# Kernel optimization log

Hardware: AMD Instinct MI355X
Metric: run time of the kernel (lower is better)

## Reference

```python
import jax, jax.numpy as jnp
import numpy as np

EPS = 1e-5
NUM_GROUPS = 32


def setup_inputs() -> dict:
    key = jax.random.key(0)
    ks = jax.random.split(key, 8)
    B, C, H, W = 4, 256, 64, 64
    cond_dim = 512
    s = 0.02
    return {
        "x": jax.random.normal(ks[0], (B, C, H, W), jnp.float32),
        "cond": jax.random.normal(ks[1], (B, cond_dim), jnp.float32),
        "lin_w": jax.random.normal(ks[2], (cond_dim, 2 * C), jnp.float32) * s,
        "lin_b": jnp.zeros((2 * C,), jnp.float32),
        "qkv_w": jax.random.normal(ks[3], (C, 3 * C), jnp.float32) * s,
        "qkv_b": jnp.zeros((3 * C,), jnp.float32),
        "proj_w": jax.random.normal(ks[4], (C, C), jnp.float32) * s,
        "proj_b": jnp.zeros((C,), jnp.float32),
    }


def _group_norm(x):
    # x: [B, C, H, W]; normalize per (batch, group) over (C/G, H, W)
    B, C, H, W = x.shape
    xg = x.reshape(B, NUM_GROUPS, C // NUM_GROUPS, H, W)
    mean = jnp.mean(xg, axis=(2, 3, 4), keepdims=True)
    var = jnp.var(xg, axis=(2, 3, 4), keepdims=True)
    xg = (xg - mean) * jax.lax.rsqrt(var + EPS)
    return xg.reshape(B, C, H, W)


def reference(x, cond, lin_w, lin_b, qkv_w, qkv_b, proj_w, proj_b):
    B, C, H, W = x.shape
    # AdaGroupNorm
    h = _group_norm(x)
    sb = cond @ lin_w + lin_b                       # [B, 2C]
    scale, bias = jnp.split(sb, 2, axis=-1)
    h = h * (1.0 + scale)[:, :, None, None] + bias[:, :, None, None]
    # tokens: [B, HW, C]
    t = h.reshape(B, C, H * W).transpose(0, 2, 1)
    qkv = t @ qkv_w + qkv_b                          # [B, HW, 3C]
    q, k, v = jnp.split(qkv, 3, axis=-1)
    attn = jnp.einsum("bnc,bmc->bnm", q, k) / jnp.sqrt(jnp.float32(C))
    attn = jax.nn.softmax(attn, axis=-1)
    o = jnp.einsum("bnm,bmc->bnc", attn, v)          # [B, HW, C]
    o = o @ proj_w + proj_b
    o = o.transpose(0, 2, 1).reshape(B, C, H, W)
    return x + o
```

## Files before the change

kernel.cpp:

```cpp
#include <hip/hip_runtime.h>
#include <stdint.h>


#define AS1 __attribute__((address_space(1)))
#define AS3 __attribute__((address_space(3)))

typedef __attribute__((ext_vector_type(8))) short bf16x8;
typedef __attribute__((ext_vector_type(16))) float f32x16;

static __device__ __forceinline__ unsigned short bf16r(float x) {
  union { float f; unsigned u; } v; v.f = x;
  return (unsigned short)((v.u + 0x7fffu + ((v.u >> 16) & 1u)) >> 16);
}
static __device__ __forceinline__ float bf2f(short x) {
  union { unsigned u; float f; } v;
  v.u = ((unsigned)(unsigned short)x) << 16;
  return v.f;
}
static __device__ __forceinline__ unsigned bf16pack(float lo, float hi) {
  union { float f; unsigned u; } a, b; a.f = lo; b.f = hi;
  unsigned ua = a.u + 0x7fffu + ((a.u >> 16) & 1u);
  unsigned ub = b.u + 0x7fffu + ((b.u >> 16) & 1u);
  return (ua >> 16) | (ub & 0xffff0000u);
}
static __device__ __forceinline__ void gload16(const void* g, void* lds_uniform) {
  __builtin_amdgcn_global_load_lds((const AS1 unsigned*)g, (AS3 unsigned*)lds_uniform,
                                   16, 0, 0);
}
static __device__ __forceinline__ f32x16 mfma_bf16(bf16x8 a, bf16x8 b, f32x16 c) {
  return __builtin_amdgcn_mfma_f32_32x32x16_bf16(a, b, c, 0, 0, 0);
}

__global__ __launch_bounds__(256) void prep_kernel(
    const float* __restrict__ qkv_w, const float* __restrict__ proj_w,
    const float* __restrict__ cond, const float* __restrict__ lin_w,
    const float* __restrict__ lin_b,
    unsigned short* __restrict__ qkvwT, unsigned short* __restrict__ projwT,
    float* __restrict__ sb) {
  int bid = blockIdx.x, t = threadIdx.x;
  if (bid < 64) {
    __shared__ float tile[64][68];
    const float* src;
    unsigned short* dst;
    int srcCols, j0, c0;
    if (bid < 48) {
      src = qkv_w; dst = qkvwT; srcCols = 768;
      j0 = (bid >> 2) * 64; c0 = (bid & 3) * 64;
    } else {
      int b2 = bid - 48;
      src = proj_w; dst = projwT; srcCols = 256;
      j0 = (b2 >> 2) * 64; c0 = (b2 & 3) * 64;
    }
    int r = t >> 4, col4 = (t & 15) * 4;
#pragma unroll
    for (int q = 0; q < 4; ++q) {
      float4 v = *(const float4*)(src + (size_t)(c0 + r + q * 16) * srcCols + j0 + col4);
      *(float4*)&tile[r + q * 16][col4] = v;
    }
    __syncthreads();
    int jj = t >> 2, cc = (t & 3) * 16;
    union { unsigned short us[16]; bf16x8 v[2]; } o;
#pragma unroll
    for (int i = 0; i < 16; ++i) o.us[i] = bf16r(tile[cc + i][jj]);
    unsigned short* dp = dst + (size_t)(j0 + jj) * 256 + c0 + cc;
    *(bf16x8*)dp = o.v[0];
    *(bf16x8*)(dp + 8) = o.v[1];
  } else {
    int s = bid - 64;
    int b = s >> 1, j = (s & 1) * 256 + t;
    float acc = lin_b[j];
    const float* cp = cond + b * 512;
    const float* wp = lin_w + j;
#pragma unroll 8
    for (int kk = 0; kk < 512; ++kk) acc += cp[kk] * wp[(size_t)kk * 512];
    sb[b * 512 + j] = acc;
  }
}

__global__ __launch_bounds__(256) void gn_stats_kernel(
    const float* __restrict__ x, float* __restrict__ stats) {
  int bg = blockIdx.x;
  const float* p = x + (size_t)bg * 32768;
  float s = 0.f, ss = 0.f;
  for (int k = 0; k < 32; ++k) {
    int i = threadIdx.x * 4 + k * 1024;
    float4 v = *(const float4*)(p + i);
    s += v.x + v.y + v.z + v.w;
    ss += v.x * v.x + v.y * v.y + v.z * v.z + v.w * v.w;
  }
#pragma unroll
  for (int off = 1; off < 64; off <<= 1) {
    s += __shfl_xor(s, off, 64);
    ss += __shfl_xor(ss, off, 64);
  }
  __shared__ float red[8];
  if ((threadIdx.x & 63) == 0) {
    red[(threadIdx.x >> 6) * 2] = s;
    red[(threadIdx.x >> 6) * 2 + 1] = ss;
  }
  __syncthreads();
  if (threadIdx.x == 0) {
    float S = 0.f, SS = 0.f;
#pragma unroll
    for (int i = 0; i < 4; ++i) { S += red[i * 2]; SS += red[i * 2 + 1]; }
    float mean = S * (1.f / 32768.f);
    float var = SS * (1.f / 32768.f) - mean * mean;
    stats[bg * 2] = mean;
    stats[bg * 2 + 1] = rsqrtf(var + 1e-5f);
  }
}

__global__ __launch_bounds__(256) void gn_apply_kernel(
    const float* __restrict__ x, const float* __restrict__ stats,
    const float* __restrict__ sb, unsigned short* __restrict__ ht) {
  __shared__ __align__(16) unsigned short tile[64][72];
  int b = blockIdx.x >> 8, cb = (blockIdx.x >> 6) & 3, nb = blockIdx.x & 63;
  int t = threadIdx.x;
  int c0 = cb * 64, n0 = nb * 64;
#pragma unroll
  for (int q = 0; q < 4; ++q) {
    int r = q * 16 + (t >> 4);
    int nn = (t & 15) * 4;
    int c = c0 + r;
    float mean = stats[(b * 32 + (c >> 3)) * 2];
    float rstd = stats[(b * 32 + (c >> 3)) * 2 + 1];
    float scl = sb[b * 512 + c], bia = sb[b * 512 + 256 + c];
    float A = rstd * (1.f + scl);
    float Bp = bia - mean * A;
    float4 v = *(const float4*)(x + ((size_t)(b * 256 + c)) * 4096 + n0 + nn);
    ushort4 pk;
    pk.x = bf16r(v.x * A + Bp);
    pk.y = bf16r(v.y * A + Bp);
    pk.z = bf16r(v.z * A + Bp);
    pk.w = bf16r(v.w * A + Bp);
    *(ushort4*)&tile[r][nn] = pk;
  }
  __syncthreads();
#pragma unroll
  for (int q = 0; q < 2; ++q) {
    int n = t & 63, cbase = (t >> 6) * 8 + q * 32;
    bf16x8 outv;
#pragma unroll
    for (int j = 0; j < 8; ++j) outv[j] = (short)tile[cbase + j][n];
    *(bf16x8*)(ht + ((size_t)(b * 4096 + n0 + n)) * 256 + c0 + cbase) = outv;
  }
}

__global__ __launch_bounds__(256, 2) void qkv_gemm_kernel(
    const unsigned short* __restrict__ ht, const unsigned short* __restrict__ wT,
    const float* __restrict__ qkv_b, unsigned short* __restrict__ q_buf,
    unsigned short* __restrict__ k_buf, unsigned short* __restrict__ vt_buf) {
  __shared__ __align__(16) unsigned short lA[8192];
  __shared__ __align__(16) unsigned short lB[8192];
  int bid = blockIdx.x;
  int b = bid / 192, rem = bid % 192;
  int m0 = (rem / 6) * 128, j0 = (rem % 6) * 128;
  int tid = threadIdx.x, lane = tid & 63, w = tid >> 6;
  int wm = w >> 1, wn = w & 1, l31 = lane & 31, lh = lane >> 5;

  f32x16 acc[2][2];
#pragma unroll
  for (int i = 0; i < 2; ++i)
#pragma unroll
    for (int jj = 0; jj < 2; ++jj) acc[i][jj] = (f32x16)0.f;

  const char* htg = (const char*)ht;
  const char* wtg = (const char*)wT;

  for (int ks = 0; ks < 4; ++ks) {
    int k0 = ks * 64;
    if (ks) __syncthreads();
#pragma unroll
    for (int i = 0; i < 4; ++i) {
      int obase = (w * 4 + i) * 1024;
      int o = obase + lane * 16;
      int row = o >> 7, colb = o & 127;
      int sw = (row & 7) << 4;
      gload16(htg + (((size_t)(b * 4096 + m0 + row)) * 256 + k0) * 2 + (colb ^ sw),
              (char*)lA + obase);
      gload16(wtg + (((size_t)(j0 + row)) * 256 + k0) * 2 + (colb ^ sw),
              (char*)lB + obase);
    }
    __syncthreads();
#pragma unroll
    for (int ks16 = 0; ks16 < 4; ++ks16) {
      int colb = ks16 * 32 + lh * 16;
      bf16x8 af[2], bf[2];
#pragma unroll
      for (int ms = 0; ms < 2; ++ms) {
        int row = wm * 64 + ms * 32 + l31;
        af[ms] = *(const bf16x8*)((const char*)lA + row * 128 + (colb ^ ((row & 7) << 4)));
      }
#pragma unroll
      for (int ns = 0; ns < 2; ++ns) {
        int row = wn * 64 + ns * 32 + l31;
        bf[ns] = *(const bf16x8*)((const char*)lB + row * 128 + (colb ^ ((row & 7) << 4)));
      }
#pragma unroll
      for (int ms = 0; ms < 2; ++ms)
#pragma unroll
        for (int ns = 0; ns < 2; ++ns) acc[ms][ns] = mfma_bf16(af[ms], bf[ns], acc[ms][ns]);
    }
  }

#pragma unroll
  for (int ms = 0; ms < 2; ++ms)
#pragma unroll
    for (int ns = 0; ns < 2; ++ns) {
      int j = j0 + wn * 64 + ns * 32 + l31;
      float bias = qkv_b[j];
      if (j < 512) {
        unsigned short* dst = (j < 256) ? q_buf : k_buf;
        int jj = j & 255;
#pragma unroll
        for (int r = 0; r < 16; ++r) {
          int mrow = m0 + wm * 64 + ms * 32 + (r & 3) + 8 * (r >> 2) + 4 * lh;
          dst[((size_t)(b * 4096) + mrow) * 256 + jj] = bf16r(acc[ms][ns][r] + bias);
        }
      } else {
        int d = j - 512;
#pragma unroll
        for (int qd = 0; qd < 4; ++qd) {
          int nbase = m0 + wm * 64 + ms * 32 + 8 * qd + 4 * lh;
          ushort4 pk;
          pk.x = bf16r(acc[ms][ns][qd * 4 + 0] + bias);
          pk.y = bf16r(acc[ms][ns][qd * 4 + 1] + bias);
          pk.z = bf16r(acc[ms][ns][qd * 4 + 2] + bias);
          pk.w = bf16r(acc[ms][ns][qd * 4 + 3] + bias);
          *(ushort4*)(vt_buf + ((size_t)(b * 256) + d) * 4096 + nbase) = pk;
        }
      }
    }
}

__global__ __launch_bounds__(512, 2) void flash_kernel(
    const unsigned short* __restrict__ qb, const unsigned short* __restrict__ kb,
    const unsigned short* __restrict__ vtb, unsigned short* __restrict__ op0,
    unsigned short* __restrict__ op1, float* __restrict__ lbuf) {
  __shared__ __align__(16) char lds[131072];
  int bid = blockIdx.x;
  int b = (bid & 7) >> 1;
  int kvh = bid & 1;
  int qt = bid >> 3;
  int tid = threadIdx.x, lane = tid & 63, w = tid >> 6;
  int wq = w & 3, wk = w >> 2;
  int l31 = lane & 31, lh = lane >> 5;
  const size_t bq = (size_t)b * 4096;
  const int qrow = qt * 128 + wq * 32 + l31;

  bf16x8 qf[16];
  const unsigned short* qp = qb + (bq + qrow) * 256;
#pragma unroll
  for (int f = 0; f < 16; ++f) qf[f] = *(const bf16x8*)(qp + f * 16 + lh * 8);

  f32x16 oacc[8];
#pragma unroll
  for (int dt = 0; dt < 8; ++dt) oacc[dt] = (f32x16)0.f;
  float l = 0.f;

  const char* kg = (const char*)(kb + (bq + (size_t)kvh * 2048) * 256);
  const char* vg = (const char*)(vtb + (size_t)b * 1048576 + (size_t)kvh * 2048);
  const float sc = 0.09016844f;

  auto STAGE = [&](int bufsel, int it2) {
    char* base = lds + bufsel * 65536;
    int key0 = it2 * 64;
#pragma unroll
    for (int i = 0; i < 8; ++i) {
      int obase = w * 8192 + i * 1024;
      int o = obase + lane * 16;
      if (w < 4) {
        int row = o >> 9, colb = o & 511;
        gload16(kg + (size_t)(key0 + row) * 512 + (colb ^ ((row & 7) << 4)),
                base + obase);
      } else {
        int vo = o - 32768;
        int rd = vo >> 7, cb2 = vo & 127;
        gload16(vg + (size_t)rd * 8192 + key0 * 2 + (cb2 ^ ((rd & 7) << 4)),
                base + obase);
      }
    }
  };

  STAGE(0, 0);
  __syncthreads();

  for (int it = 0; it < 32; ++it) {
    int cur = it & 1;
    if (it < 31) STAGE(cur ^ 1, it + 1);
    char* kbase = lds + cur * 65536;
    char* vbase = kbase + 32768;

    f32x16 sa = (f32x16)0.f;
#pragma unroll
    for (int cc = 0; cc < 16; ++cc) {
      int row = wk * 32 + l31;
      int colb = cc * 32 + lh * 16;
      bf16x8 af = *(const bf16x8*)(kbase + row * 512 + (colb ^ ((row & 7) << 4)));
      sa = mfma_bf16(af, qf[cc], sa);
    }

    float pv[16];
    float rs = 0.f;
#pragma unroll
    for (int r = 0; r < 16; ++r) {
      pv[r] = exp2f(fmaf(sa[r], sc, -8.0f));
      rs += pv[r];
    }
    rs += __shfl_xor(rs, 32, 64);
    l += rs;

    unsigned pk[8], rcv[4];
#pragma unroll
    for (int q = 0; q < 8; ++q) pk[q] = bf16pack(pv[2 * q], pv[2 * q + 1]);
    {
      const int m0s[4] = {0, 1, 4, 5}, m1s[4] = {2, 3, 6, 7};
#pragma unroll
      for (int i = 0; i < 4; ++i) {
        unsigned send = lh ? pk[m0s[i]] : pk[m1s[i]];
        rcv[i] = (unsigned)__shfl_xor((int)send, 32, 64);
      }
    }
    bf16x8 pa[2];
#pragma unroll
    for (int kk = 0; kk < 2; ++kk) {
      union { unsigned u[4]; bf16x8 v; } fr;
      if (lh == 0) {
        fr.u[0] = pk[kk * 4];     fr.u[1] = pk[kk * 4 + 1];
        fr.u[2] = rcv[kk * 2];    fr.u[3] = rcv[kk * 2 + 1];
      } else {
        fr.u[0] = rcv[kk * 2];    fr.u[1] = rcv[kk * 2 + 1];
        fr.u[2] = pk[kk * 4 + 2]; fr.u[3] = pk[kk * 4 + 3];
      }
      pa[kk] = fr.v;
    }

#pragma unroll
    for (int dt = 0; dt < 8; ++dt) {
      int rowd = dt * 32 + l31;
      int sw = (rowd & 7) << 4;
#pragma unroll
      for (int kk = 0; kk < 2; ++kk) {
        int colb = wk * 64 + kk * 32 + lh * 16;
        bf16x8 vf = *(const bf16x8*)(vbase + rowd * 128 + (colb ^ sw));
        oacc[dt] = mfma_bf16(pa[kk], vf, oacc[dt]);
      }
    }
    __syncthreads();
  }

  float* red = (float*)lds;
  if (lane < 32) red[w * 32 + l31] = l;
  __syncthreads();
  float ltot = l + red[(w ^ 4) * 32 + l31];
  __syncthreads();

  float* obuf = (float*)lds;
  if (wk == 0) {
#pragma unroll
    for (int dt = 0; dt < 8; ++dt)
#pragma unroll
      for (int r = 0; r < 16; ++r) {
        int rr = (r & 3) + 8 * (r >> 2) + 4 * lh;
        obuf[(wq * 32 + rr) * 256 + dt * 32 + l31] = oacc[dt][r];
      }
  }
  __syncthreads();
  if (wk == 1) {
    unsigned short* op = kvh ? op1 : op0;
#pragma unroll
    for (int dt = 0; dt < 8; ++dt)
#pragma unroll
      for (int r = 0; r < 16; ++r) {
        int rr = (r & 3) + 8 * (r >> 2) + 4 * lh;
        float v = oacc[dt][r] + obuf[(wq * 32 + rr) * 256 + dt * 32 + l31];
        op[(bq + qt * 128 + wq * 32 + rr) * 256 + dt * 32 + l31] = bf16r(v);
      }
    if (lane < 32) lbuf[kvh * 16384 + bq + qt * 128 + wq * 32 + l31] = ltot;
  }
}

__global__ __launch_bounds__(256) void flash_merge_kernel(
    const unsigned short* __restrict__ op0, const unsigned short* __restrict__ op1,
    const float* __restrict__ lbuf, unsigned short* __restrict__ ob) {
  int g = blockIdx.x * 256 + threadIdx.x;
  int e0 = g * 8;
  int row = e0 >> 8;
  float inv = 1.f / (lbuf[row] + lbuf[16384 + row]);
  bf16x8 a = *(const bf16x8*)(op0 + e0);
  bf16x8 c = *(const bf16x8*)(op1 + e0);
  union { unsigned short us[8]; bf16x8 v; } o;
#pragma unroll
  for (int j = 0; j < 8; ++j)
    o.us[j] = bf16r((bf2f(a[j]) + bf2f(c[j])) * inv);
  *(bf16x8*)(ob + e0) = o.v;
}

__global__ __launch_bounds__(256, 2) void proj_gemm_kernel(
    const unsigned short* __restrict__ obf, const unsigned short* __restrict__ wT,
    const float* __restrict__ proj_b, const float* __restrict__ x,
    float* __restrict__ out) {
  __shared__ __align__(16) unsigned short lA[8192];
  __shared__ __align__(16) unsigned short lB[8192];
  int bid = blockIdx.x;
  int b = bid >> 6, mt = (bid >> 1) & 31, nt = bid & 1;
  int m0 = mt * 128, j0 = nt * 128;
  int tid = threadIdx.x, lane = tid & 63, w = tid >> 6;
  int wm = w >> 1, wn = w & 1, l31 = lane & 31, lh = lane >> 5;

  f32x16 acc[2][2];
#pragma unroll
  for (int i = 0; i < 2; ++i)
#pragma unroll
    for (int jj = 0; jj < 2; ++jj) acc[i][jj] = (f32x16)0.f;

  const char* og = (const char*)obf;
  const char* wtg = (const char*)wT;

  for (int ks = 0; ks < 4; ++ks) {
    int k0 = ks * 64;
    if (ks) __syncthreads();
#pragma unroll
    for (int i = 0; i < 4; ++i) {
      int obase = (w * 4 + i) * 1024;
      int o = obase + lane * 16;
      int row = o >> 7, colb = o & 127;
      int sw = (row & 7) << 4;
      gload16(og + (((size_t)(b * 4096 + m0 + row)) * 256 + k0) * 2 + (colb ^ sw),
              (char*)lA + obase);
      gload16(wtg + (((size_t)(j0 + row)) * 256 + k0) * 2 + (colb ^ sw),
              (char*)lB + obase);
    }
    __syncthreads();
#pragma unroll
    for (int ks16 = 0; ks16 < 4; ++ks16) {
      int colb = ks16 * 32 + lh * 16;
      bf16x8 af[2], bf[2];
#pragma unroll
      for (int ms = 0; ms < 2; ++ms) {
        int row = wm * 64 + ms * 32 + l31;
        af[ms] = *(const bf16x8*)((const char*)lA + row * 128 + (colb ^ ((row & 7) << 4)));
      }
#pragma unroll
      for (int ns = 0; ns < 2; ++ns) {
        int row = wn * 64 + ns * 32 + l31;
        bf[ns] = *(const bf16x8*)((const char*)lB + row * 128 + (colb ^ ((row & 7) << 4)));
      }
#pragma unroll
      for (int ms = 0; ms < 2; ++ms)
#pragma unroll
        for (int ns = 0; ns < 2; ++ns) acc[ms][ns] = mfma_bf16(af[ms], bf[ns], acc[ms][ns]);
    }
  }

#pragma unroll
  for (int ms = 0; ms < 2; ++ms)
#pragma unroll
    for (int ns = 0; ns < 2; ++ns) {
      int j = j0 + wn * 64 + ns * 32 + l31;
      float bias = proj_b[j];
#pragma unroll
      for (int qd = 0; qd < 4; ++qd) {
        int nbase = m0 + wm * 64 + ms * 32 + 8 * qd + 4 * lh;
        size_t off = ((size_t)(b * 256) + j) * 4096 + nbase;
        float4 xr = *(const float4*)(x + off);
        float4 o4;
        o4.x = xr.x + bias + acc[ms][ns][qd * 4 + 0];
        o4.y = xr.y + bias + acc[ms][ns][qd * 4 + 1];
        o4.z = xr.z + bias + acc[ms][ns][qd * 4 + 2];
        o4.w = xr.w + bias + acc[ms][ns][qd * 4 + 3];
        *(float4*)(out + off) = o4;
      }
    }
}

extern "C" void kernel_launch(void* const* d_in, const int* in_sizes, int n_in,
                              void* d_out, int out_size, void* d_ws, size_t ws_size,
                              hipStream_t stream) {
  (void)in_sizes; (void)n_in; (void)out_size; (void)ws_size;
  const float* x      = (const float*)d_in[0];
  const float* cond   = (const float*)d_in[1];
  const float* lin_w  = (const float*)d_in[2];
  const float* lin_b  = (const float*)d_in[3];
  const float* qkv_w  = (const float*)d_in[4];
  const float* qkv_b  = (const float*)d_in[5];
  const float* proj_w = (const float*)d_in[6];
  const float* proj_b = (const float*)d_in[7];
  float* out = (float*)d_out;
  char* ws = (char*)d_ws;

  float* sb              = (float*)(ws + 0);
  float* stats           = (float*)(ws + 8192);
  unsigned short* qkvwT  = (unsigned short*)(ws + 16384);
  unsigned short* projwT = (unsigned short*)(ws + 409600);
  unsigned short* ht     = (unsigned short*)(ws + 540672);
  unsigned short* op0    = ht;
  unsigned short* q_buf  = (unsigned short*)(ws + 8929280);
  unsigned short* ob     = q_buf;
  unsigned short* k_buf  = (unsigned short*)(ws + 17317888);
  unsigned short* vt_buf = (unsigned short*)(ws + 25706496);
  unsigned short* op1    = (unsigned short*)(ws + 34095104);
  float* lbuf            = (float*)(ws + 42483712);

  prep_kernel<<<72, 256, 0, stream>>>(qkv_w, proj_w, cond, lin_w, lin_b,
                                      qkvwT, projwT, sb);
  gn_stats_kernel<<<128, 256, 0, stream>>>(x, stats);
  gn_apply_kernel<<<1024, 256, 0, stream>>>(x, stats, sb, ht);
  qkv_gemm_kernel<<<768, 256, 0, stream>>>(ht, qkvwT, qkv_b, q_buf, k_buf, vt_buf);
  flash_kernel<<<256, 512, 0, stream>>>(q_buf, k_buf, vt_buf, op0, op1, lbuf);
  flash_merge_kernel<<<2048, 256, 0, stream>>>(op0, op1, lbuf, ob);
  proj_gemm_kernel<<<256, 256, 0, stream>>>(ob, projwT, proj_b, x, out);
}
```

Measured before the change: 339.0 us.

## Split flash attention KV into four blocks and pre-tile V in MFMA order

The flash kernel now splits the key/value sequence four ways across separate 256-thread blocks, so 512 blocks run instead of 256 blocks of 512 threads. This removes the in-block LDS reduction between two key-half wavegroups. The QKV GEMM writes V in a chunked layout that matches the MFMA fragment order, so staging becomes a contiguous copy and LDS reads need no swizzle. The merge kernel now sums four bf16 partials, which adds global traffic and rounding for those partials.

```diff
diff --git a/kernel.cpp b/kernel.cpp
--- a/kernel.cpp
+++ b/kernel.cpp
@@ -149,7 +149,7 @@
 __global__ __launch_bounds__(256, 2) void qkv_gemm_kernel(
     const unsigned short* __restrict__ ht, const unsigned short* __restrict__ wT,
     const float* __restrict__ qkv_b, unsigned short* __restrict__ q_buf,
-    unsigned short* __restrict__ k_buf, unsigned short* __restrict__ vt_buf) {
+    unsigned short* __restrict__ k_buf, unsigned short* __restrict__ vtc) {
   __shared__ __align__(16) unsigned short lA[8192];
   __shared__ __align__(16) unsigned short lB[8192];
   int bid = blockIdx.x;
@@ -221,32 +221,34 @@
         int d = j - 512;
 #pragma unroll
         for (int qd = 0; qd < 4; ++qd) {
-          int nbase = m0 + wm * 64 + ms * 32 + 8 * qd + 4 * lh;
+          int n = m0 + wm * 64 + ms * 32 + 8 * qd + 4 * lh;
           ushort4 pk;
           pk.x = bf16r(acc[ms][ns][qd * 4 + 0] + bias);
           pk.y = bf16r(acc[ms][ns][qd * 4 + 1] + bias);
           pk.z = bf16r(acc[ms][ns][qd * 4 + 2] + bias);
           pk.w = bf16r(acc[ms][ns][qd * 4 + 3] + bias);
-          *(ushort4*)(vt_buf + ((size_t)(b * 256) + d) * 4096 + nbase) = pk;
+          size_t addr = (size_t)(b * 128 + (n >> 5)) * 8192 +
+                        (size_t)((n >> 3) & 3) * 2048 + d * 8 + (n & 7);
+          *(ushort4*)(vtc + addr) = pk;
         }
       }
     }
 }
 
-__global__ __launch_bounds__(512, 2) void flash_kernel(
+__global__ __launch_bounds__(256, 2) void flash_kernel(
     const unsigned short* __restrict__ qb, const unsigned short* __restrict__ kb,
-    const unsigned short* __restrict__ vtb, unsigned short* __restrict__ op0,
-    unsigned short* __restrict__ op1, float* __restrict__ lbuf) {
-  __shared__ __align__(16) char lds[131072];
+    const unsigned short* __restrict__ vtc, unsigned short* __restrict__ op0,
+    unsigned short* __restrict__ op1, unsigned short* __restrict__ op2,
+    unsigned short* __restrict__ op3, float* __restrict__ lbuf) {
+  __shared__ __align__(16) char lds[65536];
   int bid = blockIdx.x;
-  int b = (bid & 7) >> 1;
-  int kvh = bid & 1;
-  int qt = bid >> 3;
+  int kvh = bid & 3;
+  int b = (bid >> 2) & 3;
+  int qt = bid >> 4;
   int tid = threadIdx.x, lane = tid & 63, w = tid >> 6;
-  int wq = w & 3, wk = w >> 2;
   int l31 = lane & 31, lh = lane >> 5;
   const size_t bq = (size_t)b * 4096;
-  const int qrow = qt * 128 + wq * 32 + l31;
+  const int qrow = qt * 128 + w * 32 + l31;
 
   bf16x8 qf[16];
   const unsigned short* qp = qb + (bq + qrow) * 256;
@@ -258,26 +260,23 @@
   for (int dt = 0; dt < 8; ++dt) oacc[dt] = (f32x16)0.f;
   float l = 0.f;
 
-  const char* kg = (const char*)(kb + (bq + (size_t)kvh * 2048) * 256);
-  const char* vg = (const char*)(vtb + (size_t)b * 1048576 + (size_t)kvh * 2048);
+  const char* kg = (const char*)(kb + (bq + (size_t)kvh * 1024) * 256);
+  const char* vg = (const char*)vtc + ((size_t)(b * 128 + kvh * 32)) * 16384;
   const float sc = 0.09016844f;
 
   auto STAGE = [&](int bufsel, int it2) {
-    char* base = lds + bufsel * 65536;
-    int key0 = it2 * 64;
+    char* base = lds + bufsel * 32768;
+    int key0 = it2 * 32;
 #pragma unroll
     for (int i = 0; i < 8; ++i) {
-      int obase = w * 8192 + i * 1024;
-      int o = obase + lane * 16;
-      if (w < 4) {
+      if (w < 2) {
+        int o = (w * 8 + i) * 1024 + lane * 16;
         int row = o >> 9, colb = o & 511;
         gload16(kg + (size_t)(key0 + row) * 512 + (colb ^ ((row & 7) << 4)),
-                base + obase);
+                base + o);
       } else {
-        int vo = o - 32768;
-        int rd = vo >> 7, cb2 = vo & 127;
-        gload16(vg + (size_t)rd * 8192 + key0 * 2 + (cb2 ^ ((rd & 7) << 4)),
-                base + obase);
+        int vo = ((w - 2) * 8 + i) * 1024 + lane * 16;
+        gload16(vg + (size_t)it2 * 16384 + vo, base + 16384 + vo);
       }
     }
   };
@@ -288,15 +287,14 @@
   for (int it = 0; it < 32; ++it) {
     int cur = it & 1;
     if (it < 31) STAGE(cur ^ 1, it + 1);
-    char* kbase = lds + cur * 65536;
-    char* vbase = kbase + 32768;
+    char* kbase = lds + cur * 32768;
+    char* vbase = kbase + 16384;
 
     f32x16 sa = (f32x16)0.f;
 #pragma unroll
     for (int cc = 0; cc < 16; ++cc) {
-      int row = wk * 32 + l31;
-      int colb = cc * 32 + lh * 16;
-      bf16x8 af = *(const bf16x8*)(kbase + row * 512 + (colb ^ ((row & 7) << 4)));
+      bf16x8 af = *(const bf16x8*)(kbase + l31 * 512 +
+                                   ((cc * 32 + lh * 16) ^ ((l31 & 7) << 4)));
       sa = mfma_bf16(af, qf[cc], sa);
     }
 
@@ -337,62 +335,44 @@
 
 #pragma unroll
     for (int dt = 0; dt < 8; ++dt) {
-      int rowd = dt * 32 + l31;
-      int sw = (rowd & 7) << 4;
 #pragma unroll
       for (int kk = 0; kk < 2; ++kk) {
-        int colb = wk * 64 + kk * 32 + lh * 16;
-        bf16x8 vf = *(const bf16x8*)(vbase + rowd * 128 + (colb ^ sw));
+        bf16x8 vf = *(const bf16x8*)(vbase + (kk * 2 + lh) * 4096 +
+                                     (dt * 32 + l31) * 16);
         oacc[dt] = mfma_bf16(pa[kk], vf, oacc[dt]);
       }
     }
     __syncthreads();
   }
 
-  float* red = (float*)lds;
-  if (lane < 32) red[w * 32 + l31] = l;
-  __syncthreads();
-  float ltot = l + red[(w ^ 4) * 32 + l31];
-  __syncthreads();
-
-  float* obuf = (float*)lds;
-  if (wk == 0) {
-#pragma unroll
-    for (int dt = 0; dt < 8; ++dt)
-#pragma unroll
-      for (int r = 0; r < 16; ++r) {
-        int rr = (r & 3) + 8 * (r >> 2) + 4 * lh;
-        obuf[(wq * 32 + rr) * 256 + dt * 32 + l31] = oacc[dt][r];
-      }
-  }
-  __syncthreads();
-  if (wk == 1) {
-    unsigned short* op = kvh ? op1 : op0;
-#pragma unroll
-    for (int dt = 0; dt < 8; ++dt)
-#pragma unroll
-      for (int r = 0; r < 16; ++r) {
-        int rr = (r & 3) + 8 * (r >> 2) + 4 * lh;
-        float v = oacc[dt][r] + obuf[(wq * 32 + rr) * 256 + dt * 32 + l31];
-        op[(bq + qt * 128 + wq * 32 + rr) * 256 + dt * 32 + l31] = bf16r(v);
-      }
-    if (lane < 32) lbuf[kvh * 16384 + bq + qt * 128 + wq * 32 + l31] = ltot;
-  }
+  unsigned short* op = (kvh == 0) ? op0 : (kvh == 1) ? op1 : (kvh == 2) ? op2 : op3;
+#pragma unroll
+  for (int dt = 0; dt < 8; ++dt)
+#pragma unroll
+    for (int r = 0; r < 16; ++r) {
+      int rr = (r & 3) + 8 * (r >> 2) + 4 * lh;
+      op[(bq + qt * 128 + w * 32 + rr) * 256 + dt * 32 + l31] = bf16r(oacc[dt][r]);
+    }
+  if (lane < 32) lbuf[kvh * 16384 + bq + qt * 128 + w * 32 + l31] = l;
 }
 
 __global__ __launch_bounds__(256) void flash_merge_kernel(
     const unsigned short* __restrict__ op0, const unsigned short* __restrict__ op1,
+    const unsigned short* __restrict__ op2, const unsigned short* __restrict__ op3,
     const float* __restrict__ lbuf, unsigned short* __restrict__ ob) {
   int g = blockIdx.x * 256 + threadIdx.x;
   int e0 = g * 8;
   int row = e0 >> 8;
-  float inv = 1.f / (lbuf[row] + lbuf[16384 + row]);
+  float inv = 1.f / (lbuf[row] + lbuf[16384 + row] + lbuf[32768 + row] +
+                     lbuf[49152 + row]);
   bf16x8 a = *(const bf16x8*)(op0 + e0);
   bf16x8 c = *(const bf16x8*)(op1 + e0);
+  bf16x8 d = *(const bf16x8*)(op2 + e0);
+  bf16x8 e = *(const bf16x8*)(op3 + e0);
   union { unsigned short us[8]; bf16x8 v; } o;
 #pragma unroll
   for (int j = 0; j < 8; ++j)
-    o.us[j] = bf16r((bf2f(a[j]) + bf2f(c[j])) * inv);
+    o.us[j] = bf16r((bf2f(a[j]) + bf2f(c[j]) + bf2f(d[j]) + bf2f(e[j])) * inv);
   *(bf16x8*)(ob + e0) = o.v;
 }
 
@@ -498,16 +478,18 @@
   unsigned short* q_buf  = (unsigned short*)(ws + 8929280);
   unsigned short* ob     = q_buf;
   unsigned short* k_buf  = (unsigned short*)(ws + 17317888);
-  unsigned short* vt_buf = (unsigned short*)(ws + 25706496);
+  unsigned short* vtc    = (unsigned short*)(ws + 25706496);
   unsigned short* op1    = (unsigned short*)(ws + 34095104);
-  float* lbuf            = (float*)(ws + 42483712);
+  unsigned short* op2    = (unsigned short*)(ws + 42483712);
+  unsigned short* op3    = (unsigned short*)(ws + 50872320);
+  float* lbuf            = (float*)(ws + 59260928);
 
   prep_kernel<<<72, 256, 0, stream>>>(qkv_w, proj_w, cond, lin_w, lin_b,
                                       qkvwT, projwT, sb);
   gn_stats_kernel<<<128, 256, 0, stream>>>(x, stats);
   gn_apply_kernel<<<1024, 256, 0, stream>>>(x, stats, sb, ht);
-  qkv_gemm_kernel<<<768, 256, 0, stream>>>(ht, qkvwT, qkv_b, q_buf, k_buf, vt_buf);
-  flash_kernel<<<256, 512, 0, stream>>>(q_buf, k_buf, vt_buf, op0, op1, lbuf);
-  flash_merge_kernel<<<2048, 256, 0, stream>>>(op0, op1, lbuf, ob);
+  qkv_gemm_kernel<<<768, 256, 0, stream>>>(ht, qkvwT, qkv_b, q_buf, k_buf, vtc);
+  flash_kernel<<<512, 256, 0, stream>>>(q_buf, k_buf, vtc, op0, op1, op2, op3, lbuf);
+  flash_merge_kernel<<<2048, 256, 0, stream>>>(op0, op1, op2, op3, lbuf, ob);
   proj_gemm_kernel<<<256, 256, 0, stream>>>(ob, projwT, proj_b, x, out);
 }
```

Result: faster. 310.2 us (-8.5%).
